# Performance work log

Hardware: AMD Instinct MI355X
Metric: run time of the kernel (lower is better)

## Reference

```python
import jax, jax.numpy as jnp
import numpy as np
import math

D_MODEL = 768
H = 12
D_K = D_MODEL // H
KSIZE = 3  # 2*suppression_radius+1


def setup_inputs() -> dict:
    key = jax.random.key(0)
    ks = jax.random.split(key, 12)
    B, S = 8, 1024
    s = 1.0 / math.sqrt(D_MODEL)
    return {
        "q": jax.random.normal(ks[0], (B, S, D_MODEL), jnp.float32),
        "k": jax.random.normal(ks[1], (B, S, D_MODEL), jnp.float32),
        "v": jax.random.normal(ks[2], (B, S, D_MODEL), jnp.float32),
        "wq": jax.random.normal(ks[3], (D_MODEL, D_MODEL), jnp.float32) * s,
        "bq": jnp.zeros((D_MODEL,), jnp.float32),
        "wk": jax.random.normal(ks[4], (D_MODEL, D_MODEL), jnp.float32) * s,
        "bk": jnp.zeros((D_MODEL,), jnp.float32),
        "wv": jax.random.normal(ks[5], (D_MODEL, D_MODEL), jnp.float32) * s,
        "bv": jnp.zeros((D_MODEL,), jnp.float32),
        "wo": jax.random.normal(ks[6], (D_MODEL, D_MODEL), jnp.float32) * s,
        "bo": jnp.zeros((D_MODEL,), jnp.float32),
        "conv_w": jax.random.normal(ks[7], (H, 1, KSIZE, KSIZE), jnp.float32) * 0.1,
    }


def reference(q, k, v, wq, bq, wk, bk, wv, bv, wo, bo, conv_w):
    B, S, _ = q.shape
    # projections -> [B, h, S, d_k]
    Q = (q @ wq.T + bq).reshape(B, S, H, D_K).transpose(0, 2, 1, 3)
    K = (k @ wk.T + bk).reshape(B, S, H, D_K).transpose(0, 2, 1, 3)
    V = (v @ wv.T + bv).reshape(B, S, H, D_K).transpose(0, 2, 1, 3)
    scale = 1.0 / math.sqrt(D_K)
    scores = jnp.einsum("bhqd,bhkd->bhqk", Q, K) * scale  # [B,h,S,S]
    # per-head depthwise 3x3 conv over the score "image" (SAME padding, no bias)
    supp = jax.lax.conv_general_dilated(
        scores, conv_w, window_strides=(1, 1), padding="SAME",
        dimension_numbers=("NCHW", "OIHW", "NCHW"), feature_group_count=H)
    probs = jax.nn.softmax(scores - supp, axis=-1)
    out = jnp.einsum("bhqk,bhkd->bhqd", probs, V)
    out = out.transpose(0, 2, 1, 3).reshape(B, S, D_MODEL)
    return out @ wo.T + bo
```

## Files before the change

### kernel.cpp

```cpp
#include <hip/hip_runtime.h>
#include <math.h>

typedef __attribute__((ext_vector_type(8))) short short8;
typedef __attribute__((ext_vector_type(4))) float f32x4;
typedef __attribute__((ext_vector_type(4))) unsigned short ushort4v;

#define D_MODEL 768
#define NH      12
#define DK      64
#define SEQ     1024
#define NB      8
#define MTOT    (NB*SEQ)
#define NELT    ((size_t)MTOT*D_MODEL)
#define WELT    ((size_t)D_MODEL*D_MODEL)
#define L2E     1.44269504088896f

__device__ __forceinline__ unsigned short f2bf(float f) {
    unsigned int u = __builtin_bit_cast(unsigned int, f);
    unsigned int r = (u + 0x7FFFu + ((u >> 16) & 1u)) >> 16;
    return (unsigned short)r;
}
__device__ __forceinline__ float bf2f(unsigned short h) {
    return __builtin_bit_cast(float, ((unsigned int)h) << 16);
}
__device__ __forceinline__ float fast_exp2(float x) {
#if __has_builtin(__builtin_amdgcn_exp2f)
    return __builtin_amdgcn_exp2f(x);
#else
    return __expf(x * 0.69314718056f);
#endif
}
__device__ __forceinline__ unsigned int pk_bf16_rn(float lo, float hi) {
    unsigned int ul = __builtin_bit_cast(unsigned int, lo) + 0x8000u;
    unsigned int uh = __builtin_bit_cast(unsigned int, hi) + 0x8000u;
    return __builtin_amdgcn_perm(uh, ul, 0x07060302u);
}
__device__ __forceinline__ void gload_lds16(const void* g, void* lds) {
    __builtin_amdgcn_global_load_lds(
        (const __attribute__((address_space(1))) unsigned int*)g,
        (__attribute__((address_space(3))) unsigned int*)lds, 16, 0, 0);
}

__global__ __launch_bounds__(256) void cvt_all(
    const float* __restrict__ q, const float* __restrict__ k, const float* __restrict__ v,
    const float* __restrict__ wq, const float* __restrict__ wk,
    const float* __restrict__ wv, const float* __restrict__ wo,
    unsigned short* __restrict__ qb, unsigned short* __restrict__ kb, unsigned short* __restrict__ vb,
    unsigned short* __restrict__ wqb, unsigned short* __restrict__ wkb,
    unsigned short* __restrict__ wvb, unsigned short* __restrict__ wob)
{
    size_t i = (size_t)blockIdx.x * 256 + threadIdx.x;
    const size_t per = NELT / 8, wper = WELT / 8;
    const float* s; unsigned short* d; size_t l;
    if (i < per)            { s = q;  d = qb;  l = i; }
    else if (i < 2*per)     { s = k;  d = kb;  l = i - per; }
    else if (i < 3*per)     { s = v;  d = vb;  l = i - 2*per; }
    else {
        size_t j = i - 3*per;
        if (j < wper)        { s = wq; d = wqb; l = j; }
        else if (j < 2*wper) { s = wk; d = wkb; l = j - wper; }
        else if (j < 3*wper) { s = wv; d = wvb; l = j - 2*wper; }
        else                 { s = wo; d = wob; l = j - 3*wper; }
    }
    const float4* sp = (const float4*)(s + l*8);
    float4 v0 = sp[0], v1 = sp[1];
    short8 o;
    o[0]=(short)f2bf(v0.x); o[1]=(short)f2bf(v0.y); o[2]=(short)f2bf(v0.z); o[3]=(short)f2bf(v0.w);
    o[4]=(short)f2bf(v1.x); o[5]=(short)f2bf(v1.y); o[6]=(short)f2bf(v1.z); o[7]=(short)f2bf(v1.w);
    *(short8*)(d + l*8) = o;
}

#define BM 128
#define BN 128
#define BKG 64

__global__ __launch_bounds__(256) void proj_gemm(
    const unsigned short* __restrict__ Aq, const unsigned short* __restrict__ Ak,
    const unsigned short* __restrict__ Av,
    const unsigned short* __restrict__ Wq, const unsigned short* __restrict__ Wk,
    const unsigned short* __restrict__ Wv,
    const float* __restrict__ bq, const float* __restrict__ bk, const float* __restrict__ bv,
    unsigned short* __restrict__ Qp, unsigned short* __restrict__ Kp,
    unsigned short* __restrict__ Vtp)
{
    __shared__ unsigned short As[BM*BKG];
    __shared__ unsigned short Bs[BN*BKG];
    const int tid = threadIdx.x;
    const int lane = tid & 63, wid = tid >> 6;
    const int wr = wid >> 1, wc = wid & 1;
    const int m0 = blockIdx.y * BM, n0 = blockIdx.x * BN;
    const int z = blockIdx.z;

    const unsigned short* A = (z == 0) ? Aq : (z == 1) ? Ak : Av;
    const unsigned short* W = (z == 0) ? Wq : (z == 1) ? Wk : Wv;
    const float* bias       = (z == 0) ? bq : (z == 1) ? bk : bv;

    f32x4 acc[4][4];
    #pragma unroll
    for (int i = 0; i < 4; ++i)
        #pragma unroll
        for (int j = 0; j < 4; ++j) acc[i][j] = (f32x4)(0.f);

    for (int k0 = 0; k0 < D_MODEL; k0 += BKG) {
        __syncthreads();
        #pragma unroll
        for (int j = 0; j < 4; ++j) {
            int p = ((wid*4 + j) << 9) + lane*8;
            int row = p >> 6, off = p & 63;
            const unsigned short* srcA = A + (size_t)(m0+row)*D_MODEL + k0 + (off ^ ((row&7)<<3));
            gload_lds16(srcA, &As[(wid*4 + j) << 9]);
            const unsigned short* srcB = W + (size_t)(n0+row)*D_MODEL + k0 + (off ^ ((row&7)<<3));
            gload_lds16(srcB, &Bs[(wid*4 + j) << 9]);
        }
        __syncthreads();
        #pragma unroll
        for (int ks = 0; ks < 2; ++ks) {
            short8 af[4], bf8[4];
            #pragma unroll
            for (int mi = 0; mi < 4; ++mi) {
                int row = wr*64 + mi*16 + (lane & 15);
                af[mi] = *(const short8*)&As[row*BKG + ((ks*32 + (lane>>4)*8) ^ ((row&7)<<3))];
            }
            #pragma unroll
            for (int ni = 0; ni < 4; ++ni) {
                int row = wc*64 + ni*16 + (lane & 15);
                bf8[ni] = *(const short8*)&Bs[row*BKG + ((ks*32 + (lane>>4)*8) ^ ((row&7)<<3))];
            }
            #pragma unroll
            for (int mi = 0; mi < 4; ++mi)
                #pragma unroll
                for (int ni = 0; ni < 4; ++ni)
                    acc[mi][ni] = __builtin_amdgcn_mfma_f32_16x16x32_bf16(af[mi], bf8[ni], acc[mi][ni], 0, 0, 0);
        }
    }

    float bv4[4];
    #pragma unroll
    for (int ni = 0; ni < 4; ++ni) bv4[ni] = bias[n0 + wc*64 + ni*16 + (lane & 15)];

    if (z < 2) {
        unsigned short* C = (z == 0) ? Qp : Kp;
        const float scale = (z == 0) ? 0.125f : 1.0f;
        #pragma unroll
        for (int mi = 0; mi < 4; ++mi)
            #pragma unroll
            for (int ni = 0; ni < 4; ++ni) {
                int col = n0 + wc*64 + ni*16 + (lane & 15);
                int rbase = m0 + wr*64 + mi*16 + ((lane>>4)<<2);
                #pragma unroll
                for (int j = 0; j < 4; ++j)
                    C[(size_t)(rbase+j)*D_MODEL + col] = f2bf((acc[mi][ni][j] + bv4[ni]) * scale);
            }
    } else {
        #pragma unroll
        for (int mi = 0; mi < 4; ++mi)
            #pragma unroll
            for (int ni = 0; ni < 4; ++ni) {
                int col = n0 + wc*64 + ni*16 + (lane & 15);
                int hh = col >> 6, dd = col & 63;
                int m = m0 + wr*64 + mi*16 + ((lane>>4)<<2);
                int bb = m >> 10, ss = m & (SEQ-1);
                ushort4v pk;
                #pragma unroll
                for (int j = 0; j < 4; ++j) pk[j] = f2bf(acc[mi][ni][j] + bv4[ni]);
                *(ushort4v*)&Vtp[((size_t)(bb*NH + hh)*DK + dd)*SEQ + ss] = pk;
            }
    }
}

__global__ __launch_bounds__(256) void gemm_out(
    const unsigned short* __restrict__ A, const unsigned short* __restrict__ W,
    const float* __restrict__ bias, float* __restrict__ C)
{
    __shared__ unsigned short As[BM*BKG];
    __shared__ unsigned short Bs[BN*BKG];
    const int tid = threadIdx.x;
    const int lane = tid & 63, wid = tid >> 6;
    const int wr = wid >> 1, wc = wid & 1;
    const int m0 = blockIdx.y * BM, n0 = blockIdx.x * BN;

    f32x4 acc[4][4];
    #pragma unroll
    for (int i = 0; i < 4; ++i)
        #pragma unroll
        for (int j = 0; j < 4; ++j) acc[i][j] = (f32x4)(0.f);

    for (int k0 = 0; k0 < D_MODEL; k0 += BKG) {
        __syncthreads();
        #pragma unroll
        for (int j = 0; j < 4; ++j) {
            int p = ((wid*4 + j) << 9) + lane*8;
            int row = p >> 6, off = p & 63;
            const unsigned short* srcA = A + (size_t)(m0+row)*D_MODEL + k0 + (off ^ ((row&7)<<3));
            gload_lds16(srcA, &As[(wid*4 + j) << 9]);
            const unsigned short* srcB = W + (size_t)(n0+row)*D_MODEL + k0 + (off ^ ((row&7)<<3));
            gload_lds16(srcB, &Bs[(wid*4 + j) << 9]);
        }
        __syncthreads();
        #pragma unroll
        for (int ks = 0; ks < 2; ++ks) {
            short8 af[4], bf8[4];
            #pragma unroll
            for (int mi = 0; mi < 4; ++mi) {
                int row = wr*64 + mi*16 + (lane & 15);
                af[mi] = *(const short8*)&As[row*BKG + ((ks*32 + (lane>>4)*8) ^ ((row&7)<<3))];
            }
            #pragma unroll
            for (int ni = 0; ni < 4; ++ni) {
                int row = wc*64 + ni*16 + (lane & 15);
                bf8[ni] = *(const short8*)&Bs[row*BKG + ((ks*32 + (lane>>4)*8) ^ ((row&7)<<3))];
            }
            #pragma unroll
            for (int mi = 0; mi < 4; ++mi)
                #pragma unroll
                for (int ni = 0; ni < 4; ++ni)
                    acc[mi][ni] = __builtin_amdgcn_mfma_f32_16x16x32_bf16(af[mi], bf8[ni], acc[mi][ni], 0, 0, 0);
        }
    }

    float bv4[4];
    #pragma unroll
    for (int ni = 0; ni < 4; ++ni) bv4[ni] = bias[n0 + wc*64 + ni*16 + (lane & 15)];

    #pragma unroll
    for (int mi = 0; mi < 4; ++mi)
        #pragma unroll
        for (int ni = 0; ni < 4; ++ni) {
            int col = n0 + wc*64 + ni*16 + (lane & 15);
            int rbase = m0 + wr*64 + mi*16 + ((lane>>4)<<2);
            #pragma unroll
            for (int j = 0; j < 4; ++j)
                C[(size_t)(rbase+j)*D_MODEL + col] = acc[mi][ni][j] + bv4[ni];
        }
}

#define KVB 64
#define NCH (SEQ/KVB)
#define THR 8.0f

__global__ __launch_bounds__(512, 4) void attn_flash(
    const unsigned short* __restrict__ Qp,
    const unsigned short* __restrict__ Kp,
    const unsigned short* __restrict__ Vt,
    const float* __restrict__ CW,
    unsigned short* __restrict__ Aop)
{
    __shared__ unsigned short Ks[2][66*64];
    __shared__ unsigned short Vs[2][64*64];
    __shared__ unsigned short UB[130*64];

    const int tid = threadIdx.x;
    const int lane = tid & 63, wid = tid >> 6;
    const int lq = lane & 15, lg = lane >> 4;

    const int bid = blockIdx.x;
    const int sw = (bid & 7) * 96 + (bid >> 3);
    const int q0 = (sw & 7) * 128;
    const int bh = sw >> 3;
    const int h = bh % NH, b = bh / NH;

    float wcv[9];
    #pragma unroll
    for (int i = 0; i < 9; ++i) wcv[i] = CW[h*9 + i];

    const unsigned short* KpB = Kp + (size_t)b*SEQ*D_MODEL + h*DK;
    const unsigned short* QpB = Qp + (size_t)b*SEQ*D_MODEL + h*DK;
    const char* VtB = (const char*)Vt + (size_t)bh*DK*SEQ*2;

    short8 kr0, kr1;
    auto kload = [&](int ck) {
        { int r = tid >> 3, oct = tid & 7;
          int gk = ck*KVB - 1 + r;
          short8 v = (short8)0;
          if (gk >= 0 && gk < SEQ) v = *(const short8*)&KpB[(size_t)gk*D_MODEL + oct*8];
          kr0 = v; }
        if (tid < 16) {
          int r = 64 + (tid >> 3), oct = tid & 7;
          int gk = ck*KVB - 1 + r;
          short8 v = (short8)0;
          if (gk >= 0 && gk < SEQ) v = *(const short8*)&KpB[(size_t)gk*D_MODEL + oct*8];
          kr1 = v; }
    };
    auto kstore = [&](int buf) {
        { int r = tid >> 3, oct = tid & 7;
          *(short8*)&Ks[buf][r*64 + ((oct ^ (r&7)) << 3)] = kr0; }
        if (tid < 16) {
          int r = 64 + (tid >> 3), oct = tid & 7;
          *(short8*)&Ks[buf][r*64 + ((oct ^ (r&7)) << 3)] = kr1; }
    };
    auto vstage = [&](int ck, int buf) {
        int p = tid * 16;
        int row = p >> 7, off = p & 127;
        const char* src = VtB + ((size_t)row*SEQ + ck*KVB)*2 + (off ^ ((row&7)<<4));
        gload_lds16(src, (char*)Vs[buf] + p);
    };

    kload(0);

    {
        short8 qs0 = (short8)0, qs1 = (short8)0, qs2 = (short8)0;
        int r0 = tid >> 3, o0 = tid & 7;
        int g0 = q0 - 1 + r0;
        if (g0 >= 0 && g0 < SEQ) qs0 = *(const short8*)&QpB[(size_t)g0*D_MODEL + o0*8];
        int r1 = (512 + tid) >> 3, o1 = tid & 7;
        int g1 = q0 - 1 + r1;
        if (g1 >= 0 && g1 < SEQ) qs1 = *(const short8*)&QpB[(size_t)g1*D_MODEL + o1*8];
        int r2 = 0, o2 = 0, g2 = -1;
        if (tid < 16) {
            r2 = (1024 + tid) >> 3; o2 = tid & 7;
            g2 = q0 - 1 + r2;
            if (g2 >= 0 && g2 < SEQ) qs2 = *(const short8*)&QpB[(size_t)g2*D_MODEL + o2*8];
        }
        *(short8*)&UB[r0*64 + ((o0 ^ (r0&7)) << 3)] = qs0;
        *(short8*)&UB[r1*64 + ((o1 ^ (r1&7)) << 3)] = qs1;
        if (tid < 16) *(short8*)&UB[r2*64 + ((o2 ^ (r2&7)) << 3)] = qs2;
    }
    __syncthreads();

    short8 qtf0[2], qtf1[2], qtf2[2];
    {
        int r0 = wid*16 + lq;
        #pragma unroll
        for (int ks = 0; ks < 2; ++ks) {
            int oct = ks*4 + lg;
            int ra = r0, rb = r0 + 1, rc = r0 + 2;
            short8 am = *(const short8*)&UB[ra*64 + ((oct ^ (ra&7)) << 3)];
            short8 ac = *(const short8*)&UB[rb*64 + ((oct ^ (rb&7)) << 3)];
            short8 ap = *(const short8*)&UB[rc*64 + ((oct ^ (rc&7)) << 3)];
            short8 f0, f1, f2;
            #pragma unroll
            for (int j = 0; j < 8; ++j) {
                float fm = bf2f((unsigned short)am[j]);
                float fc = bf2f((unsigned short)ac[j]);
                float fp = bf2f((unsigned short)ap[j]);
                float t0 = (fc - (wcv[1]*fm + wcv[4]*fc + wcv[7]*fp)) * L2E;
                float t1 = -(wcv[0]*fm + wcv[3]*fc + wcv[6]*fp) * L2E;
                float t2 = -(wcv[2]*fm + wcv[5]*fc + wcv[8]*fp) * L2E;
                f0[j] = (short)f2bf(t0);
                f1[j] = (short)f2bf(t1);
                f2[j] = (short)f2bf(t2);
            }
            qtf0[ks] = f0; qtf1[ks] = f1; qtf2[ks] = f2;
        }
    }
    kstore(0);
    vstage(0, 0);
    __syncthreads();

    unsigned short* Pw = &UB[wid * 1024];

    float m = -1e30f, l = 0.f;
    f32x4 oac[4];
    #pragma unroll
    for (int dt = 0; dt < 4; ++dt) oac[dt] = (f32x4)(0.f);

    int cur = 0;
    for (int ck = 0; ck < NCH; ++ck) {
        if (ck < NCH-1) { kload(ck+1); vstage(ck+1, cur^1); }

        f32x4 st[4];
        #pragma unroll
        for (int t = 0; t < 4; ++t) {
            f32x4 s = (f32x4)(0.f);
            #pragma unroll
            for (int ks = 0; ks < 2; ++ks) {
                int oct = ks*4 + lg;
                int ar0 = t*16 + lq + 1;
                short8 a0 = *(const short8*)&Ks[cur][ar0*64 + ((oct ^ (ar0&7)) << 3)];
                s = __builtin_amdgcn_mfma_f32_16x16x32_bf16(a0, qtf0[ks], s, 0, 0, 0);
                int ar1 = t*16 + lq;
                short8 a1 = *(const short8*)&Ks[cur][ar1*64 + ((oct ^ (ar1&7)) << 3)];
                s = __builtin_amdgcn_mfma_f32_16x16x32_bf16(a1, qtf1[ks], s, 0, 0, 0);
                int ar2 = t*16 + lq + 2;
                short8 a2 = *(const short8*)&Ks[cur][ar2*64 + ((oct ^ (ar2&7)) << 3)];
                s = __builtin_amdgcn_mfma_f32_16x16x32_bf16(a2, qtf2[ks], s, 0, 0, 0);
            }
            st[t] = s;
        }

        float tmax = -1e30f;
        #pragma unroll
        for (int t = 0; t < 4; ++t)
            #pragma unroll
            for (int j = 0; j < 4; ++j) tmax = fmaxf(tmax, st[t][j]);
        tmax = fmaxf(tmax, __shfl_xor(tmax, 16));
        tmax = fmaxf(tmax, __shfl_xor(tmax, 32));

        if (!__all(tmax - m <= THR)) {
            float mn = fmaxf(m, tmax);
            float r = fast_exp2(m - mn);
            l *= r;
            #pragma unroll
            for (int dt = 0; dt < 4; ++dt)
                #pragma unroll
                for (int j = 0; j < 4; ++j) oac[dt][j] *= r;
            m = mn;
        }
        float lsum = 0.f;
        #pragma unroll
        for (int t = 0; t < 4; ++t)
            #pragma unroll
            for (int j = 0; j < 4; ++j) {
                float e = fast_exp2(st[t][j] - m);
                st[t][j] = e;
                lsum += e;
            }
        lsum += __shfl_xor(lsum, 16);
        lsum += __shfl_xor(lsum, 32);
        l += lsum;

        #pragma unroll
        for (int t = 0; t < 4; ++t) {
            uint2 pk;
            pk.x = pk_bf16_rn(st[t][0], st[t][1]);
            pk.y = pk_bf16_rn(st[t][2], st[t][3]);
            *(uint2*)&Pw[lq*64 + ((t*16 + lg*4) ^ ((lq&7)<<3))] = pk;
        }
        #pragma unroll
        for (int kk = 0; kk < 2; ++kk) {
            short8 p8 = *(const short8*)&Pw[lq*64 + ((kk*32 + lg*8) ^ ((lq&7)<<3))];
            #pragma unroll
            for (int dt = 0; dt < 4; ++dt) {
                int vr = dt*16 + lq;
                int voct = kk*4 + lg;
                short8 v8 = *(const short8*)&Vs[cur][vr*64 + ((voct ^ (vr&7)) << 3)];
                oac[dt] = __builtin_amdgcn_mfma_f32_16x16x32_bf16(v8, p8, oac[dt], 0, 0, 0);
            }
        }

        if (ck < NCH-1) kstore(cur^1);
        __syncthreads();
        cur ^= 1;
    }

    float invl = 1.0f / l;
    int qg = q0 + wid*16 + lq;
    #pragma unroll
    for (int dt = 0; dt < 4; ++dt) {
        uint2 o;
        o.x = pk_bf16_rn(oac[dt][0] * invl, oac[dt][1] * invl);
        o.y = pk_bf16_rn(oac[dt][2] * invl, oac[dt][3] * invl);
        *(uint2*)&Aop[(size_t)(b*SEQ + qg)*D_MODEL + h*DK + dt*16 + lg*4] = o;
    }
}

extern "C" void kernel_launch(void* const* d_in, const int* in_sizes, int n_in,
                              void* d_out, int out_size, void* d_ws, size_t ws_size,
                              hipStream_t stream)
{
    const float* q  = (const float*)d_in[0];
    const float* k  = (const float*)d_in[1];
    const float* v  = (const float*)d_in[2];
    const float* wq = (const float*)d_in[3];
    const float* bq = (const float*)d_in[4];
    const float* wk = (const float*)d_in[5];
    const float* bk = (const float*)d_in[6];
    const float* wv = (const float*)d_in[7];
    const float* bv = (const float*)d_in[8];
    const float* wo = (const float*)d_in[9];
    const float* bo = (const float*)d_in[10];
    const float* cw = (const float*)d_in[11];

    unsigned short* qb  = (unsigned short*)d_ws;
    unsigned short* kb  = qb  + NELT;
    unsigned short* vb  = kb  + NELT;
    unsigned short* wqb = vb  + NELT;
    unsigned short* wkb = wqb + WELT;
    unsigned short* wvb = wkb + WELT;
    unsigned short* wob = wvb + WELT;
    unsigned short* Qp  = wob + WELT;
    unsigned short* Kp  = Qp  + NELT;
    unsigned short* Vtp = Kp  + NELT;
    unsigned short* Aop = Vtp + NELT;

    const int cvtBlocks = (int)((3*NELT + 4*WELT) / 8 / 256);
    cvt_all<<<cvtBlocks, 256, 0, stream>>>(q, k, v, wq, wk, wv, wo,
                                           qb, kb, vb, wqb, wkb, wvb, wob);

    dim3 gg(D_MODEL/BN, MTOT/BM, 3);
    proj_gemm<<<gg, 256, 0, stream>>>(qb, kb, vb, wqb, wkb, wvb, bq, bk, bv, Qp, Kp, Vtp);

    attn_flash<<<dim3(768), 512, 0, stream>>>(Qp, Kp, Vtp, cw, Aop);

    gemm_out<<<dim3(D_MODEL/BN, MTOT/BM), 256, 0, stream>>>(Aop, wob, bo, (float*)d_out);
}
```

Baseline: 163.2 us.

## Switch attention to 32x32 MFMA tiles with permlane P reshuffle, 4 waves

The attention kernel now uses 32x32x16 bf16 MFMAs with 4 waves of 32 query rows each, instead of 16x16x32 MFMAs with 8 waves of 16 rows. The probability tile is rearranged in registers with permlane32_swap rather than written to and read back from a per-wave LDS scratch buffer. Q rows are loaded straight from global memory, which removes the UB staging buffer and one barrier. In exchange the kernel uses more registers per wave and fewer waves per block (launch bounds 256,3), which may reduce latency hiding.

```diff
diff --git a/kernel.cpp b/kernel.cpp
--- a/kernel.cpp
+++ b/kernel.cpp
@@ -3,7 +3,9 @@
 
 typedef __attribute__((ext_vector_type(8))) short short8;
 typedef __attribute__((ext_vector_type(4))) float f32x4;
+typedef __attribute__((ext_vector_type(16))) float f32x16;
 typedef __attribute__((ext_vector_type(4))) unsigned short ushort4v;
+typedef __attribute__((ext_vector_type(4))) unsigned int u32x4;
 
 #define D_MODEL 768
 #define NH      12
@@ -34,6 +36,18 @@
     unsigned int ul = __builtin_bit_cast(unsigned int, lo) + 0x8000u;
     unsigned int uh = __builtin_bit_cast(unsigned int, hi) + 0x8000u;
     return __builtin_amdgcn_perm(uh, ul, 0x07060302u);
+}
+__device__ __forceinline__ void plswap(unsigned int &a, unsigned int &b, int g) {
+#if __has_builtin(__builtin_amdgcn_permlane32_swap)
+    typedef __attribute__((ext_vector_type(2))) unsigned int uint2v;
+    uint2v r = __builtin_amdgcn_permlane32_swap(a, b, false, false);
+    a = r[0]; b = r[1];
+#else
+    unsigned int sa = __shfl_xor(a, 32), sb = __shfl_xor(b, 32);
+    unsigned int na = g ? sb : a;
+    unsigned int nb = g ? b : sa;
+    a = na; b = nb;
+#endif
 }
 __device__ __forceinline__ void gload_lds16(const void* g, void* lds) {
     __builtin_amdgcn_global_load_lds(
@@ -238,7 +252,7 @@
 #define NCH (SEQ/KVB)
 #define THR 8.0f
 
-__global__ __launch_bounds__(512, 4) void attn_flash(
+__global__ __launch_bounds__(256, 3) void attn_flash(
     const unsigned short* __restrict__ Qp,
     const unsigned short* __restrict__ Kp,
     const unsigned short* __restrict__ Vt,
@@ -247,11 +261,10 @@
 {
     __shared__ unsigned short Ks[2][66*64];
     __shared__ unsigned short Vs[2][64*64];
-    __shared__ unsigned short UB[130*64];
 
     const int tid = threadIdx.x;
     const int lane = tid & 63, wid = tid >> 6;
-    const int lq = lane & 15, lg = lane >> 4;
+    const int ql = lane & 31, g = lane >> 5;
 
     const int bid = blockIdx.x;
     const int sw = (bid & 7) * 96 + (bid >> 3);
@@ -267,72 +280,59 @@
     const unsigned short* QpB = Qp + (size_t)b*SEQ*D_MODEL + h*DK;
     const char* VtB = (const char*)Vt + (size_t)bh*DK*SEQ*2;
 
-    short8 kr0, kr1;
+    short8 kreg[3];
     auto kload = [&](int ck) {
-        { int r = tid >> 3, oct = tid & 7;
-          int gk = ck*KVB - 1 + r;
-          short8 v = (short8)0;
-          if (gk >= 0 && gk < SEQ) v = *(const short8*)&KpB[(size_t)gk*D_MODEL + oct*8];
-          kr0 = v; }
-        if (tid < 16) {
-          int r = 64 + (tid >> 3), oct = tid & 7;
-          int gk = ck*KVB - 1 + r;
-          short8 v = (short8)0;
-          if (gk >= 0 && gk < SEQ) v = *(const short8*)&KpB[(size_t)gk*D_MODEL + oct*8];
-          kr1 = v; }
+        #pragma unroll
+        for (int u = 0; u < 3; ++u) {
+            int idx = tid + u*256;
+            short8 v = (short8)0;
+            if (idx < 528) {
+                int r = idx >> 3, oct = idx & 7;
+                int gk = ck*KVB - 1 + r;
+                if (gk >= 0 && gk < SEQ)
+                    v = *(const short8*)&KpB[(size_t)gk*D_MODEL + oct*8];
+            }
+            kreg[u] = v;
+        }
     };
     auto kstore = [&](int buf) {
-        { int r = tid >> 3, oct = tid & 7;
-          *(short8*)&Ks[buf][r*64 + ((oct ^ (r&7)) << 3)] = kr0; }
-        if (tid < 16) {
-          int r = 64 + (tid >> 3), oct = tid & 7;
-          *(short8*)&Ks[buf][r*64 + ((oct ^ (r&7)) << 3)] = kr1; }
+        #pragma unroll
+        for (int u = 0; u < 3; ++u) {
+            int idx = tid + u*256;
+            if (idx < 528) {
+                int r = idx >> 3, oct = idx & 7;
+                *(short8*)&Ks[buf][r*64 + ((oct ^ (r&7)) << 3)] = kreg[u];
+            }
+        }
     };
     auto vstage = [&](int ck, int buf) {
-        int p = tid * 16;
-        int row = p >> 7, off = p & 127;
-        const char* src = VtB + ((size_t)row*SEQ + ck*KVB)*2 + (off ^ ((row&7)<<4));
-        gload_lds16(src, (char*)Vs[buf] + p);
+        #pragma unroll
+        for (int u = 0; u < 2; ++u) {
+            int p = (tid + u*256) * 16;
+            int row = p >> 7, off = p & 127;
+            const char* src = VtB + ((size_t)row*SEQ + ck*KVB)*2 + (off ^ ((row&7)<<4));
+            gload_lds16(src, (char*)Vs[buf] + p);
+        }
     };
 
     kload(0);
 
+    short8 qtf[3][4];
     {
-        short8 qs0 = (short8)0, qs1 = (short8)0, qs2 = (short8)0;
-        int r0 = tid >> 3, o0 = tid & 7;
-        int g0 = q0 - 1 + r0;
-        if (g0 >= 0 && g0 < SEQ) qs0 = *(const short8*)&QpB[(size_t)g0*D_MODEL + o0*8];
-        int r1 = (512 + tid) >> 3, o1 = tid & 7;
-        int g1 = q0 - 1 + r1;
-        if (g1 >= 0 && g1 < SEQ) qs1 = *(const short8*)&QpB[(size_t)g1*D_MODEL + o1*8];
-        int r2 = 0, o2 = 0, g2 = -1;
-        if (tid < 16) {
-            r2 = (1024 + tid) >> 3; o2 = tid & 7;
-            g2 = q0 - 1 + r2;
-            if (g2 >= 0 && g2 < SEQ) qs2 = *(const short8*)&QpB[(size_t)g2*D_MODEL + o2*8];
-        }
-        *(short8*)&UB[r0*64 + ((o0 ^ (r0&7)) << 3)] = qs0;
-        *(short8*)&UB[r1*64 + ((o1 ^ (r1&7)) << 3)] = qs1;
-        if (tid < 16) *(short8*)&UB[r2*64 + ((o2 ^ (r2&7)) << 3)] = qs2;
-    }
-    __syncthreads();
-
-    short8 qtf0[2], qtf1[2], qtf2[2];
-    {
-        int r0 = wid*16 + lq;
-        #pragma unroll
-        for (int ks = 0; ks < 2; ++ks) {
-            int oct = ks*4 + lg;
-            int ra = r0, rb = r0 + 1, rc = r0 + 2;
-            short8 am = *(const short8*)&UB[ra*64 + ((oct ^ (ra&7)) << 3)];
-            short8 ac = *(const short8*)&UB[rb*64 + ((oct ^ (rb&7)) << 3)];
-            short8 ap = *(const short8*)&UB[rc*64 + ((oct ^ (rc&7)) << 3)];
+        int gq = q0 + wid*32 + ql;
+        #pragma unroll
+        for (int i = 0; i < 4; ++i) {
+            int dwin = i*16 + g*8;
+            short8 qm = (short8)0, qc, qp8 = (short8)0;
+            if (gq > 0)      qm  = *(const short8*)&QpB[(size_t)(gq-1)*D_MODEL + dwin];
+            qc = *(const short8*)&QpB[(size_t)gq*D_MODEL + dwin];
+            if (gq < SEQ-1)  qp8 = *(const short8*)&QpB[(size_t)(gq+1)*D_MODEL + dwin];
             short8 f0, f1, f2;
             #pragma unroll
             for (int j = 0; j < 8; ++j) {
-                float fm = bf2f((unsigned short)am[j]);
-                float fc = bf2f((unsigned short)ac[j]);
-                float fp = bf2f((unsigned short)ap[j]);
+                float fm = bf2f((unsigned short)qm[j]);
+                float fc = bf2f((unsigned short)qc[j]);
+                float fp = bf2f((unsigned short)qp8[j]);
                 float t0 = (fc - (wcv[1]*fm + wcv[4]*fc + wcv[7]*fp)) * L2E;
                 float t1 = -(wcv[0]*fm + wcv[3]*fc + wcv[6]*fp) * L2E;
                 float t2 = -(wcv[2]*fm + wcv[5]*fc + wcv[8]*fp) * L2E;
@@ -340,50 +340,44 @@
                 f1[j] = (short)f2bf(t1);
                 f2[j] = (short)f2bf(t2);
             }
-            qtf0[ks] = f0; qtf1[ks] = f1; qtf2[ks] = f2;
+            qtf[0][i] = f0; qtf[1][i] = f1; qtf[2][i] = f2;
         }
     }
     kstore(0);
     vstage(0, 0);
     __syncthreads();
 
-    unsigned short* Pw = &UB[wid * 1024];
-
     float m = -1e30f, l = 0.f;
-    f32x4 oac[4];
-    #pragma unroll
-    for (int dt = 0; dt < 4; ++dt) oac[dt] = (f32x4)(0.f);
+    f32x16 oac[2];
+    oac[0] = (f32x16)(0.f); oac[1] = (f32x16)(0.f);
 
     int cur = 0;
     for (int ck = 0; ck < NCH; ++ck) {
         if (ck < NCH-1) { kload(ck+1); vstage(ck+1, cur^1); }
 
-        f32x4 st[4];
-        #pragma unroll
-        for (int t = 0; t < 4; ++t) {
-            f32x4 s = (f32x4)(0.f);
-            #pragma unroll
-            for (int ks = 0; ks < 2; ++ks) {
-                int oct = ks*4 + lg;
-                int ar0 = t*16 + lq + 1;
-                short8 a0 = *(const short8*)&Ks[cur][ar0*64 + ((oct ^ (ar0&7)) << 3)];
-                s = __builtin_amdgcn_mfma_f32_16x16x32_bf16(a0, qtf0[ks], s, 0, 0, 0);
-                int ar1 = t*16 + lq;
-                short8 a1 = *(const short8*)&Ks[cur][ar1*64 + ((oct ^ (ar1&7)) << 3)];
-                s = __builtin_amdgcn_mfma_f32_16x16x32_bf16(a1, qtf1[ks], s, 0, 0, 0);
-                int ar2 = t*16 + lq + 2;
-                short8 a2 = *(const short8*)&Ks[cur][ar2*64 + ((oct ^ (ar2&7)) << 3)];
-                s = __builtin_amdgcn_mfma_f32_16x16x32_bf16(a2, qtf2[ks], s, 0, 0, 0);
-            }
-            st[t] = s;
+        f32x16 st2[2];
+        #pragma unroll
+        for (int t = 0; t < 2; ++t) {
+            f32x16 s = (f32x16)(0.f);
+            #pragma unroll
+            for (int sl = 0; sl < 3; ++sl) {
+                const int shift = (sl == 0) ? 1 : (sl == 1) ? 0 : 2;
+                int ar = t*32 + ql + shift;
+                #pragma unroll
+                for (int i = 0; i < 4; ++i) {
+                    int oct = 2*i + g;
+                    short8 a = *(const short8*)&Ks[cur][ar*64 + ((oct ^ (ar&7)) << 3)];
+                    s = __builtin_amdgcn_mfma_f32_32x32x16_bf16(a, qtf[sl][i], s, 0, 0, 0);
+                }
+            }
+            st2[t] = s;
         }
 
         float tmax = -1e30f;
         #pragma unroll
-        for (int t = 0; t < 4; ++t)
-            #pragma unroll
-            for (int j = 0; j < 4; ++j) tmax = fmaxf(tmax, st[t][j]);
-        tmax = fmaxf(tmax, __shfl_xor(tmax, 16));
+        for (int t = 0; t < 2; ++t)
+            #pragma unroll
+            for (int j = 0; j < 16; ++j) tmax = fmaxf(tmax, st2[t][j]);
         tmax = fmaxf(tmax, __shfl_xor(tmax, 32));
 
         if (!__all(tmax - m <= THR)) {
@@ -391,40 +385,48 @@
             float r = fast_exp2(m - mn);
             l *= r;
             #pragma unroll
-            for (int dt = 0; dt < 4; ++dt)
-                #pragma unroll
-                for (int j = 0; j < 4; ++j) oac[dt][j] *= r;
+            for (int dt = 0; dt < 2; ++dt)
+                #pragma unroll
+                for (int j = 0; j < 16; ++j) oac[dt][j] *= r;
             m = mn;
         }
         float lsum = 0.f;
         #pragma unroll
-        for (int t = 0; t < 4; ++t)
-            #pragma unroll
-            for (int j = 0; j < 4; ++j) {
-                float e = fast_exp2(st[t][j] - m);
-                st[t][j] = e;
+        for (int t = 0; t < 2; ++t)
+            #pragma unroll
+            for (int j = 0; j < 16; ++j) {
+                float e = fast_exp2(st2[t][j] - m);
+                st2[t][j] = e;
                 lsum += e;
             }
-        lsum += __shfl_xor(lsum, 16);
         lsum += __shfl_xor(lsum, 32);
         l += lsum;
 
-        #pragma unroll
-        for (int t = 0; t < 4; ++t) {
-            uint2 pk;
-            pk.x = pk_bf16_rn(st[t][0], st[t][1]);
-            pk.y = pk_bf16_rn(st[t][2], st[t][3]);
-            *(uint2*)&Pw[lq*64 + ((t*16 + lg*4) ^ ((lq&7)<<3))] = pk;
-        }
-        #pragma unroll
-        for (int kk = 0; kk < 2; ++kk) {
-            short8 p8 = *(const short8*)&Pw[lq*64 + ((kk*32 + lg*8) ^ ((lq&7)<<3))];
-            #pragma unroll
-            for (int dt = 0; dt < 4; ++dt) {
-                int vr = dt*16 + lq;
-                int voct = kk*4 + lg;
-                short8 v8 = *(const short8*)&Vs[cur][vr*64 + ((voct ^ (vr&7)) << 3)];
-                oac[dt] = __builtin_amdgcn_mfma_f32_16x16x32_bf16(v8, p8, oac[dt], 0, 0, 0);
+        short8 pf[4];
+        #pragma unroll
+        for (int t = 0; t < 2; ++t) {
+            #pragma unroll
+            for (int f = 0; f < 2; ++f) {
+                const int base = f*8;
+                unsigned int x0 = pk_bf16_rn(st2[t][base+0], st2[t][base+1]);
+                unsigned int x1 = pk_bf16_rn(st2[t][base+2], st2[t][base+3]);
+                unsigned int y0 = pk_bf16_rn(st2[t][base+4], st2[t][base+5]);
+                unsigned int y1 = pk_bf16_rn(st2[t][base+6], st2[t][base+7]);
+                plswap(x0, y0, g);
+                plswap(x1, y1, g);
+                u32x4 w = {x0, x1, y0, y1};
+                pf[t*2 + f] = __builtin_bit_cast(short8, w);
+            }
+        }
+
+        #pragma unroll
+        for (int f = 0; f < 4; ++f) {
+            #pragma unroll
+            for (int dt = 0; dt < 2; ++dt) {
+                int vr = dt*32 + ql;
+                int oct = 2*f + g;
+                short8 a = *(const short8*)&Vs[cur][vr*64 + ((oct ^ (vr&7)) << 3)];
+                oac[dt] = __builtin_amdgcn_mfma_f32_32x32x16_bf16(a, pf[f], oac[dt], 0, 0, 0);
             }
         }
 
@@ -434,13 +436,18 @@
     }
 
     float invl = 1.0f / l;
-    int qg = q0 + wid*16 + lq;
-    #pragma unroll
-    for (int dt = 0; dt < 4; ++dt) {
-        uint2 o;
-        o.x = pk_bf16_rn(oac[dt][0] * invl, oac[dt][1] * invl);
-        o.y = pk_bf16_rn(oac[dt][2] * invl, oac[dt][3] * invl);
-        *(uint2*)&Aop[(size_t)(b*SEQ + qg)*D_MODEL + h*DK + dt*16 + lg*4] = o;
+    int qg = q0 + wid*32 + ql;
+    size_t obase = (size_t)(b*SEQ + qg)*D_MODEL + h*DK;
+    #pragma unroll
+    for (int dt = 0; dt < 2; ++dt) {
+        #pragma unroll
+        for (int u = 0; u < 4; ++u) {
+            int d0 = dt*32 + 8*u + 4*g;
+            ushort4v o;
+            #pragma unroll
+            for (int j = 0; j < 4; ++j) o[j] = f2bf(oac[dt][4*u + j] * invl);
+            *(ushort4v*)&Aop[obase + d0] = o;
+        }
     }
 }
 
@@ -480,7 +487,7 @@
     dim3 gg(D_MODEL/BN, MTOT/BM, 3);
     proj_gemm<<<gg, 256, 0, stream>>>(qb, kb, vb, wqb, wkb, wvb, bq, bk, bv, Qp, Kp, Vtp);
 
-    attn_flash<<<dim3(768), 512, 0, stream>>>(Qp, Kp, Vtp, cw, Aop);
+    attn_flash<<<dim3(768), 256, 0, stream>>>(Qp, Kp, Vtp, cw, Aop);
 
     gemm_out<<<dim3(D_MODEL/BN, MTOT/BM), 256, 0, stream>>>(Aop, wob, bo, (float*)d_out);
 }
```

Result: no change. 165.1 us (+1.2%).
